# Kernel tuning notes

Hardware: AMD Instinct MI355X
Metric: run time of the kernel (lower is better)

## Reference

```python
import jax, jax.numpy as jnp
import numpy as np


def _quant8(w):
    # Brevitas Int8 per-tensor weight quant: scale = max|w|/127, round, clip, dequant.
    s = jnp.max(jnp.abs(w)) / 127.0
    q = jnp.clip(jnp.round(w / s), -127.0, 127.0) * s
    # straight-through estimator (matches brevitas backward)
    return w + jax.lax.stop_gradient(q - w)


def _conv1d(x, w, b):
    # x: [B, Cin, L], w: [Cout, Cin, K]
    y = jax.lax.conv_general_dilated(x, w, window_strides=(1,), padding='VALID',
                                     dimension_numbers=('NCW', 'OIW', 'NCW'))
    return y + b[None, :, None]


def _maxpool2(x):
    B, C, L = x.shape
    L2 = L // 2
    return jnp.max(x[:, :, :2 * L2].reshape(B, C, L2, 2), axis=-1)


def _lrelu(x):
    return jnp.where(x > 0, x, 0.1 * x)


def setup_inputs() -> dict:
    key = jax.random.key(0)
    ks = jax.random.split(key, 13)
    B, C, L = 32768, 2, 128
    flat = 32 * 27  # 864, from tracing conv/pool stack at L=128
    d = {
        'x': jax.random.normal(ks[0], (B, C, L), dtype=jnp.float32),
        'w1': jax.random.normal(ks[1], (16, 2, 2), dtype=jnp.float32) * 0.3,
        'b1': jax.random.normal(ks[2], (16,), dtype=jnp.float32) * 0.05,
        'w2': jax.random.normal(ks[3], (16, 16, 3), dtype=jnp.float32) * 0.1,
        'b2': jax.random.normal(ks[4], (16,), dtype=jnp.float32) * 0.05,
        'w3': jax.random.normal(ks[5], (32, 16, 5), dtype=jnp.float32) * 0.1,
        'b3': jax.random.normal(ks[6], (32,), dtype=jnp.float32) * 0.05,
        'w4': jax.random.normal(ks[7], (32, 32, 5), dtype=jnp.float32) * 0.08,
        'b4': jax.random.normal(ks[8], (32,), dtype=jnp.float32) * 0.05,
        'wd': jax.random.normal(ks[9], (64, flat), dtype=jnp.float32) * 0.03,
        'bd': jax.random.normal(ks[10], (64,), dtype=jnp.float32) * 0.05,
        'wo': jax.random.normal(ks[11], (1, 64), dtype=jnp.float32) * 0.1,
        'bo': jax.random.normal(ks[12], (1,), dtype=jnp.float32) * 0.05,
    }
    return d


def reference(x, w1, b1, w2, b2, w3, b3, w4, b4, wd, bd, wo, bo):
    h = _lrelu(_conv1d(x, _quant8(w1), b1))        # [B,16,127]
    h = _lrelu(_conv1d(h, _quant8(w2), b2))        # [B,16,125]
    h = _maxpool2(h)                               # [B,16,62]
    h = _lrelu(_conv1d(h, _quant8(w3), b3))        # [B,32,58]
    h = _lrelu(_conv1d(h, _quant8(w4), b4))        # [B,32,54]
    h = _maxpool2(h)                               # [B,32,27]
    h = h.reshape(h.shape[0], -1)                  # [B,864]
    h = _lrelu(h @ _quant8(wd).T + bd)             # [B,64]
    return h @ _quant8(wo).T + bo                  # [B,1]
```

## Files before the change

### kernel.cpp

```cpp
#include <hip/hip_runtime.h>
#include <hip/hip_bf16.h>

typedef __hip_bfloat16 bf16;
typedef _Float16 h16;
typedef __attribute__((ext_vector_type(8))) _Float16 h16x8;
typedef __attribute__((ext_vector_type(4))) float f32x4;
typedef __attribute__((ext_vector_type(16))) float f32x16;

__device__ __forceinline__ float lrelu(float x) { return x > 0.f ? x : 0.1f * x; }
__device__ __forceinline__ float ldE(const void* p, long i, int f32) {
    return f32 ? ((const float*)p)[i] : __bfloat162float(((const bf16*)p)[i]);
}
__device__ __forceinline__ uint2 pack4(float a, float b, float c, float d) {
    union { _Float16 h[4]; uint2 u; } t;
    t.h[0] = (_Float16)a; t.h[1] = (_Float16)b; t.h[2] = (_Float16)c; t.h[3] = (_Float16)d;
    return t.u;
}
#define LDS_FENCE() asm volatile("s_waitcnt lgkmcnt(0)" ::: "memory")


__device__ __forceinline__ float qv(const void* src, int idx, float sc, int f32) {
    float w = ldE(src, idx, f32);
    float q = rintf(w / sc);
    return fminf(127.f, fmaxf(-127.f, q)) * sc;
}

__global__ void __launch_bounds__(256) quant_prep(
    const unsigned short* __restrict__ xu,
    const void* __restrict__ w1, const void* __restrict__ w2,
    const void* __restrict__ w3, const void* __restrict__ w4,
    const void* __restrict__ wd, const void* __restrict__ wo,
    const void* __restrict__ b1, const void* __restrict__ b2,
    const void* __restrict__ b3, const void* __restrict__ b4,
    const void* __restrict__ bd, const void* __restrict__ bo,
    float* __restrict__ wsf)
{
    int tid = threadIdx.x;
    int which = blockIdx.x;
    __shared__ float red[256];
    __shared__ int cnt;
    if (tid == 0) cnt = 0;
    __syncthreads();
    int bad = 0;
    for (int i = tid; i < 2048; i += 256) {
        int e = (xu[i] >> 7) & 0xFF;
        if (e >= 147) bad = 1;
    }
    atomicAdd(&cnt, bad);
    __syncthreads();
    const int f32 = (cnt > 4) ? 1 : 0;
    if (tid == 0) ((int*)wsf)[290] = f32;

    h16* wh = (h16*)(wsf + 292);

    if (which == 53) {
        if (tid < 16)        wsf[64 + tid]        = ldE(b1, tid, f32);
        else if (tid < 32)   wsf[80 + tid - 16]   = ldE(b2, tid - 16, f32);
        else if (tid < 64)   wsf[96 + tid - 32]   = ldE(b3, tid - 32, f32);
        else if (tid < 96)   wsf[128 + tid - 64]  = ldE(b4, tid - 64, f32);
        else if (tid < 160)  wsf[160 + tid - 96]  = ldE(bd, tid - 96, f32);
        else if (tid == 160) wsf[288]             = ldE(bo, 0, f32);
        return;
    }

    if (which < 48) {
        float m0 = 0.f, m1 = 0.f, m2 = 0.f, m3 = 0.f;
        for (int i = tid; i < 55296; i += 1024) {
            m0 = fmaxf(m0, fabsf(ldE(wd, i, f32)));
            m1 = fmaxf(m1, fabsf(ldE(wd, i + 256, f32)));
            m2 = fmaxf(m2, fabsf(ldE(wd, i + 512, f32)));
            m3 = fmaxf(m3, fabsf(ldE(wd, i + 768, f32)));
        }
        red[tid] = fmaxf(fmaxf(m0, m1), fmaxf(m2, m3));
        __syncthreads();
        for (int s = 128; s > 0; s >>= 1) {
            if (tid < s) red[tid] = fmaxf(red[tid], red[tid + s]);
            __syncthreads();
        }
        float sc = red[0] / 127.f;
        int e1 = (which + 1) * 1152;
        for (int e = which * 1152 + tid; e < e1; e += 256) {
            int j = e & 7, l = (e >> 3) & 63, t = e >> 9;
            int mt = t / 27, c = t - mt * 27;
            int o = mt * 16 + (l & 15);
            int k = c * 32 + ((l >> 4) & 3) * 8 + j;
            int i = k >> 5, cch = k & 31;
            wh[8704 + e] = (h16)qv(wd, o * 864 + cch * 27 + i, sc, f32);
        }
        return;
    }

    const void* src; int n;
    switch (which) {
        case 48: src = w1; n = 64;   break;
        case 49: src = w2; n = 768;  break;
        case 50: src = w3; n = 2560; break;
        case 51: src = w4; n = 5120; break;
        default: src = wo; n = 64;   break;
    }
    float m = 0.f;
    for (int i = tid; i < n; i += 256) m = fmaxf(m, fabsf(ldE(src, i, f32)));
    red[tid] = m;
    __syncthreads();
    for (int s = 128; s > 0; s >>= 1) {
        if (tid < s) red[tid] = fmaxf(red[tid], red[tid + s]);
        __syncthreads();
    }
    float sc = red[0] / 127.f;

    if (which == 48) {
        if (tid < 64) wsf[tid] = qv(src, tid, sc, f32);
    } else if (which == 52) {
        if (tid < 64) wsf[224 + tid] = qv(src, tid, sc, f32);
    } else if (which == 49) {
        for (int e = tid; e < 1024; e += 256) {
            int c = e >> 9, l = (e >> 3) & 63, j = e & 7;
            int mm = l & 15;
            int k = c * 32 + ((l >> 4) & 3) * 8 + j;
            int dk = k >> 4, ci = k & 15;
            float v = (dk < 3) ? qv(src, (mm * 16 + ci) * 3 + dk, sc, f32) : 0.f;
            wh[0 + e] = (h16)v;
        }
    } else if (which == 50) {
        for (int e = tid; e < 2560; e += 256) {
            int c = e >> 9, l = (e >> 3) & 63, j = e & 7;
            int mm = l & 31;
            int ci = ((l >> 5) & 1) * 8 + j;
            wh[1024 + e] = (h16)qv(src, (mm * 16 + ci) * 5 + c, sc, f32);
        }
    } else {
        for (int e = tid; e < 5120; e += 256) {
            int c = e >> 9, l = (e >> 3) & 63, j = e & 7;
            int mm = l & 31;
            int k = c * 16 + ((l >> 5) & 1) * 8 + j;
            int dk = k >> 5, ci = k & 31;
            wh[3584 + e] = (h16)qv(src, (mm * 32 + ci) * 5 + dk, sc, f32);
        }
    }
}

__global__ void __launch_bounds__(256, 3) qcnn_main(
    const void* __restrict__ x,
    const float* __restrict__ wsf,
    void* __restrict__ out)
{
    const int f32flag = ((const int*)wsf)[290];
    const float* qw1f = wsf;
    const float* fb1g = wsf + 64;
    const h16*  wh  = (const h16*)(wsf + 292);
    const h16*  F2g = wh;
    const h16*  F3g = wh + 1024;
    const h16*  F4g = wh + 3584;
    const h16*  FDg = wh + 8704;

    __shared__ __align__(16) h16 Uall[4][2112];
    __shared__ __align__(16) h16 Vall[4][2208];
    __shared__ __align__(16) h16 flatb[8][872];
    __shared__ float red[256];

    int tid  = threadIdx.x;
    int lane = tid & 63;
    int w    = __builtin_amdgcn_readfirstlane(tid >> 6);
    int n16  = lane & 15, kg16 = (lane >> 4) & 3;
    int n32  = lane & 31, kg32 = (lane >> 5) & 1;
    int o16  = kg16 * 4;
    h16* U = Uall[w];
    h16* V = Vall[w];
    long b0 = (long)blockIdx.x * 8;

    h16x8 a2[2], a3[5], a4[10];
#pragma unroll
    for (int c = 0; c < 2; ++c)  a2[c] = *(const h16x8*)&F2g[c * 512 + lane * 8];
#pragma unroll
    for (int c = 0; c < 5; ++c)  a3[c] = *(const h16x8*)&F3g[c * 512 + lane * 8];
#pragma unroll
    for (int c = 0; c < 10; ++c) a4[c] = *(const h16x8*)&F4g[c * 512 + lane * 8];
    f32x4 b2v = *(const f32x4*)&wsf[80 + o16];

    for (int it = 0; it < 2; ++it) {
        int slot = w * 2 + it;
        long sb = (b0 + slot) * 256;

        LDS_FENCE();
        float xl[2][4];
#pragma unroll
        for (int ci = 0; ci < 2; ++ci) {
            int rb = ci * 128;
            xl[ci][0] = ldE(x, sb + rb + lane, f32flag);
            xl[ci][1] = ldE(x, sb + rb + lane + 1, f32flag);
            xl[ci][2] = ldE(x, sb + rb + 64 + lane, f32flag);
            xl[ci][3] = ldE(x, sb + rb + 64 + ((lane + 1) & 63), f32flag);
        }
        h16x8 ra, rbv, rc, rd;
#pragma unroll
        for (int co = 0; co < 16; ++co) {
            float w00 = qw1f[co*4+0], w01 = qw1f[co*4+1], w10 = qw1f[co*4+2], w11 = qw1f[co*4+3];
            float bb = fb1g[co];
            float v0 = bb + xl[0][0]*w00 + xl[0][1]*w01 + xl[1][0]*w10 + xl[1][1]*w11;
            float v1 = bb + xl[0][2]*w00 + xl[0][3]*w01 + xl[1][2]*w10 + xl[1][3]*w11;
            v0 = lrelu(v0); v1 = lrelu(v1);
            if (co < 8) { ra[co] = (h16)v0; rc[co] = (h16)v1; }
            else        { rbv[co-8] = (h16)v0; rd[co-8] = (h16)v1; }
        }
        *(h16x8*)&U[lane * 8]        = ra;
        *(h16x8*)&U[1056 + lane * 8] = rbv;
        if (lane < 63) {
            *(h16x8*)&U[(64 + lane) * 8]        = rc;
            *(h16x8*)&U[1056 + (64 + lane) * 8] = rd;
        }
        LDS_FENCE();

#pragma unroll
        for (int t = 0; t < 8; ++t) {
            int n = t * 16 + n16;
            f32x4 acc = {0.f, 0.f, 0.f, 0.f};
#pragma unroll
            for (int c = 0; c < 2; ++c) {
                int k0 = c * 32 + kg16 * 8;
                int dk = k0 >> 4, g = (k0 & 15) >> 3;
                h16x8 bfr = *(const h16x8*)&U[g * 1056 + (n + dk) * 8];
                acc = __builtin_amdgcn_mfma_f32_16x16x32_f16(a2[c], bfr, acc, 0, 0, 0);
            }
            if (n < 125) {
                uint2 p = pack4(lrelu(acc[0] + b2v[0]), lrelu(acc[1] + b2v[1]),
                                lrelu(acc[2] + b2v[2]), lrelu(acc[3] + b2v[3]));
                *(uint2*)&V[(o16 >> 3) * 1008 + n * 8 + (o16 & 7)] = p;
            }
        }
        LDS_FENCE();

        if (lane < 62) {
#pragma unroll
            for (int g = 0; g < 2; ++g) {
                h16x8 pa = *(const h16x8*)&V[g * 1008 + (2 * lane) * 8];
                h16x8 pb = *(const h16x8*)&V[g * 1008 + (2 * lane + 1) * 8];
                h16x8 mm;
#pragma unroll
                for (int e = 0; e < 8; ++e) mm[e] = pa[e] > pb[e] ? pa[e] : pb[e];
                *(h16x8*)&U[g * 1056 + lane * 8] = mm;
            }
        }
        LDS_FENCE();

#pragma unroll
        for (int t = 0; t < 2; ++t) {
            int n = t * 32 + n32;
            f32x16 acc = {0.f,0.f,0.f,0.f,0.f,0.f,0.f,0.f,0.f,0.f,0.f,0.f,0.f,0.f,0.f,0.f};
#pragma unroll
            for (int c = 0; c < 5; ++c) {
                h16x8 bfr = *(const h16x8*)&U[kg32 * 1056 + (n + c) * 8];
                acc = __builtin_amdgcn_mfma_f32_32x32x16_f16(a3[c], bfr, acc, 0, 0, 0);
            }
#pragma unroll
            for (int g = 0; g < 4; ++g) {
                int r0 = 8 * g + 4 * kg32;
                f32x4 bv = *(const f32x4*)&wsf[96 + r0];
                if (n < 58) {
                    uint2 p = pack4(lrelu(acc[4*g+0] + bv[0]), lrelu(acc[4*g+1] + bv[1]),
                                    lrelu(acc[4*g+2] + bv[2]), lrelu(acc[4*g+3] + bv[3]));
                    *(uint2*)&V[g * 552 + n * 8 + 4 * kg32] = p;
                }
            }
        }
        LDS_FENCE();

#pragma unroll
        for (int t = 0; t < 2; ++t) {
            int n = t * 32 + n32;
            f32x16 acc = {0.f,0.f,0.f,0.f,0.f,0.f,0.f,0.f,0.f,0.f,0.f,0.f,0.f,0.f,0.f,0.f};
#pragma unroll
            for (int c = 0; c < 10; ++c) {
                int k0 = c * 16 + kg32 * 8;
                int dk = k0 >> 5, g = (k0 >> 3) & 3;
                h16x8 bfr = *(const h16x8*)&V[g * 552 + (n + dk) * 8];
                acc = __builtin_amdgcn_mfma_f32_32x32x16_f16(a4[c], bfr, acc, 0, 0, 0);
            }
#pragma unroll
            for (int g = 0; g < 4; ++g) {
                int r0 = 8 * g + 4 * kg32;
                f32x4 bv = *(const f32x4*)&wsf[128 + r0];
                if (n < 54) {
                    uint2 p = pack4(lrelu(acc[4*g+0] + bv[0]), lrelu(acc[4*g+1] + bv[1]),
                                    lrelu(acc[4*g+2] + bv[2]), lrelu(acc[4*g+3] + bv[3]));
                    *(uint2*)&U[g * 448 + n * 8 + 4 * kg32] = p;
                }
            }
        }
        LDS_FENCE();

        if (lane < 27) {
#pragma unroll
            for (int g = 0; g < 4; ++g) {
                h16x8 pa = *(const h16x8*)&U[g * 448 + (2 * lane) * 8];
                h16x8 pb = *(const h16x8*)&U[g * 448 + (2 * lane + 1) * 8];
                h16x8 mm;
#pragma unroll
                for (int e = 0; e < 8; ++e) mm[e] = pa[e] > pb[e] ? pa[e] : pb[e];
                *(h16x8*)&flatb[slot][(g * 27 + lane) * 8] = mm;
            }
        }
    }
    __syncthreads();

    f32x4 dacc = {0.f, 0.f, 0.f, 0.f};
    for (int c = 0; c < 27; ++c) {
        h16x8 aw = *(const h16x8*)&FDg[((w * 27 + c) * 64 + lane) * 8];
        h16x8 bh = *(const h16x8*)&flatb[lane & 7][(kg16 * 27 + c) * 8];
        dacc = __builtin_amdgcn_mfma_f32_16x16x32_f16(aw, bh, dacc, 0, 0, 0);
    }
    int o0g = w * 16 + o16;
    f32x4 bdv = *(const f32x4*)&wsf[160 + o0g];
    f32x4 qov = *(const f32x4*)&wsf[224 + o0g];
    float part = 0.f;
#pragma unroll
    for (int q = 0; q < 4; ++q) part += lrelu(dacc[q] + bdv[q]) * qov[q];
    red[tid] = part;
    __syncthreads();
    if (tid < 8) {
        float y = wsf[288];
#pragma unroll
        for (int g = 0; g < 16; ++g) y += red[(g >> 2) * 64 + (g & 3) * 16 + tid];
        if (f32flag) ((float*)out)[b0 + tid] = y;
        else         ((bf16*)out)[b0 + tid] = __float2bfloat16(y);
    }
}

extern "C" void kernel_launch(void* const* d_in, const int* in_sizes, int n_in,
                              void* d_out, int out_size, void* d_ws, size_t ws_size,
                              hipStream_t stream) {
    const void* x  = d_in[0];
    const void* w1 = d_in[1];
    const void* b1 = d_in[2];
    const void* w2 = d_in[3];
    const void* b2 = d_in[4];
    const void* w3 = d_in[5];
    const void* b3 = d_in[6];
    const void* w4 = d_in[7];
    const void* b4 = d_in[8];
    const void* wd = d_in[9];
    const void* bd = d_in[10];
    const void* wo = d_in[11];
    const void* bo = d_in[12];
    float* wsf = (float*)d_ws;

    int B = in_sizes[0] / 256;
    quant_prep<<<54, 256, 0, stream>>>((const unsigned short*)x,
                                       w1, w2, w3, w4, wd, wo,
                                       b1, b2, b3, b4, bd, bo, wsf);
    qcnn_main<<<B / 8, 256, 0, stream>>>(x, wsf, d_out);
}
```

Before: 209.8 us.

## Fold biases into MFMA accumulators, preload inputs, and vectorize prep absmax

Initializes MFMA accumulators with the bias values so the per-element bias adds in the conv and dense epilogues go away. Rewrites leaky ReLU as a single fmax. Hoists the input loads for both iterations ahead of the loop so global latency overlaps. The prep kernel now computes absmax with vectorized integer bit-masking, and the w3/w4 quantization is split across more blocks. The costs are more live registers in the main kernel and redundant absmax reductions across the split prep blocks.

After: 214.9 us. 2.5% more time.

```diff
diff --git a/kernel.cpp b/kernel.cpp
--- a/kernel.cpp
+++ b/kernel.cpp
@@ -7,7 +7,7 @@
 typedef __attribute__((ext_vector_type(4))) float f32x4;
 typedef __attribute__((ext_vector_type(16))) float f32x16;
 
-__device__ __forceinline__ float lrelu(float x) { return x > 0.f ? x : 0.1f * x; }
+__device__ __forceinline__ float lrelu(float x) { return fmaxf(x, 0.1f * x); }
 __device__ __forceinline__ float ldE(const void* p, long i, int f32) {
     return f32 ? ((const float*)p)[i] : __bfloat162float(((const bf16*)p)[i]);
 }
@@ -16,6 +16,7 @@
     t.h[0] = (_Float16)a; t.h[1] = (_Float16)b; t.h[2] = (_Float16)c; t.h[3] = (_Float16)d;
     return t.u;
 }
+__device__ __forceinline__ unsigned umx(unsigned a, unsigned b) { return a > b ? a : b; }
 #define LDS_FENCE() asm volatile("s_waitcnt lgkmcnt(0)" ::: "memory")
 
 
@@ -25,7 +26,40 @@
     return fminf(127.f, fmaxf(-127.f, q)) * sc;
 }
 
-__global__ void __launch_bounds__(256) quant_prep(
+__device__ float block_scale(const void* src, int n, int f32, int tid, float* red) {
+    unsigned m = 0;
+    const uint4* p = (const uint4*)src;
+    if (f32) {
+        int nv = n >> 2;
+        for (int i = tid; i < nv; i += 256) {
+            uint4 u = p[i];
+            m = umx(m, u.x & 0x7FFFFFFFu); m = umx(m, u.y & 0x7FFFFFFFu);
+            m = umx(m, u.z & 0x7FFFFFFFu); m = umx(m, u.w & 0x7FFFFFFFu);
+        }
+        union { unsigned u; float f; } c; c.u = m;
+        red[tid] = c.f;
+    } else {
+        int nv = n >> 3;
+        for (int i = tid; i < nv; i += 256) {
+            uint4 u = p[i];
+            unsigned a;
+            a = u.x & 0x7FFF7FFFu; m = umx(m, a >> 16); m = umx(m, a & 0xFFFFu);
+            a = u.y & 0x7FFF7FFFu; m = umx(m, a >> 16); m = umx(m, a & 0xFFFFu);
+            a = u.z & 0x7FFF7FFFu; m = umx(m, a >> 16); m = umx(m, a & 0xFFFFu);
+            a = u.w & 0x7FFF7FFFu; m = umx(m, a >> 16); m = umx(m, a & 0xFFFFu);
+        }
+        union { unsigned u; float f; } c; c.u = m << 16;
+        red[tid] = c.f;
+    }
+    __syncthreads();
+    for (int s = 128; s > 0; s >>= 1) {
+        if (tid < s) red[tid] = fmaxf(red[tid], red[tid + s]);
+        __syncthreads();
+    }
+    return red[0] / 127.f;
+}
+
+__global__ void __launch_bounds__(256) prep(
     const unsigned short* __restrict__ xu,
     const void* __restrict__ w1, const void* __restrict__ w2,
     const void* __restrict__ w3, const void* __restrict__ w4,
@@ -35,8 +69,7 @@
     const void* __restrict__ bd, const void* __restrict__ bo,
     float* __restrict__ wsf)
 {
-    int tid = threadIdx.x;
-    int which = blockIdx.x;
+    int tid = threadIdx.x, which = blockIdx.x;
     __shared__ float red[256];
     __shared__ int cnt;
     if (tid == 0) cnt = 0;
@@ -49,35 +82,10 @@
     atomicAdd(&cnt, bad);
     __syncthreads();
     const int f32 = (cnt > 4) ? 1 : 0;
-    if (tid == 0) ((int*)wsf)[290] = f32;
-
     h16* wh = (h16*)(wsf + 292);
 
-    if (which == 53) {
-        if (tid < 16)        wsf[64 + tid]        = ldE(b1, tid, f32);
-        else if (tid < 32)   wsf[80 + tid - 16]   = ldE(b2, tid - 16, f32);
-        else if (tid < 64)   wsf[96 + tid - 32]   = ldE(b3, tid - 32, f32);
-        else if (tid < 96)   wsf[128 + tid - 64]  = ldE(b4, tid - 64, f32);
-        else if (tid < 160)  wsf[160 + tid - 96]  = ldE(bd, tid - 96, f32);
-        else if (tid == 160) wsf[288]             = ldE(bo, 0, f32);
-        return;
-    }
-
     if (which < 48) {
-        float m0 = 0.f, m1 = 0.f, m2 = 0.f, m3 = 0.f;
-        for (int i = tid; i < 55296; i += 1024) {
-            m0 = fmaxf(m0, fabsf(ldE(wd, i, f32)));
-            m1 = fmaxf(m1, fabsf(ldE(wd, i + 256, f32)));
-            m2 = fmaxf(m2, fabsf(ldE(wd, i + 512, f32)));
-            m3 = fmaxf(m3, fabsf(ldE(wd, i + 768, f32)));
-        }
-        red[tid] = fmaxf(fmaxf(m0, m1), fmaxf(m2, m3));
-        __syncthreads();
-        for (int s = 128; s > 0; s >>= 1) {
-            if (tid < s) red[tid] = fmaxf(red[tid], red[tid + s]);
-            __syncthreads();
-        }
-        float sc = red[0] / 127.f;
+        float sc = block_scale(wd, 55296, f32, tid, red);
         int e1 = (which + 1) * 1152;
         for (int e = which * 1152 + tid; e < e1; e += 256) {
             int j = e & 7, l = (e >> 3) & 63, t = e >> 9;
@@ -87,55 +95,48 @@
             int i = k >> 5, cch = k & 31;
             wh[8704 + e] = (h16)qv(wd, o * 864 + cch * 27 + i, sc, f32);
         }
-        return;
-    }
-
-    const void* src; int n;
-    switch (which) {
-        case 48: src = w1; n = 64;   break;
-        case 49: src = w2; n = 768;  break;
-        case 50: src = w3; n = 2560; break;
-        case 51: src = w4; n = 5120; break;
-        default: src = wo; n = 64;   break;
-    }
-    float m = 0.f;
-    for (int i = tid; i < n; i += 256) m = fmaxf(m, fabsf(ldE(src, i, f32)));
-    red[tid] = m;
-    __syncthreads();
-    for (int s = 128; s > 0; s >>= 1) {
-        if (tid < s) red[tid] = fmaxf(red[tid], red[tid + s]);
-        __syncthreads();
-    }
-    float sc = red[0] / 127.f;
-
-    if (which == 48) {
-        if (tid < 64) wsf[tid] = qv(src, tid, sc, f32);
-    } else if (which == 52) {
-        if (tid < 64) wsf[224 + tid] = qv(src, tid, sc, f32);
+    } else if (which == 48) {
+        float sc = block_scale(w1, 64, f32, tid, red);
+        if (tid < 64) wsf[tid] = qv(w1, tid, sc, f32);
     } else if (which == 49) {
+        float sc = block_scale(w2, 768, f32, tid, red);
         for (int e = tid; e < 1024; e += 256) {
             int c = e >> 9, l = (e >> 3) & 63, j = e & 7;
             int mm = l & 15;
             int k = c * 32 + ((l >> 4) & 3) * 8 + j;
             int dk = k >> 4, ci = k & 15;
-            float v = (dk < 3) ? qv(src, (mm * 16 + ci) * 3 + dk, sc, f32) : 0.f;
+            float v = (dk < 3) ? qv(w2, (mm * 16 + ci) * 3 + dk, sc, f32) : 0.f;
             wh[0 + e] = (h16)v;
         }
-    } else if (which == 50) {
-        for (int e = tid; e < 2560; e += 256) {
+    } else if (which < 52) {
+        float sc = block_scale(w3, 2560, f32, tid, red);
+        int e0 = (which - 50) * 1280;
+        for (int e = e0 + tid; e < e0 + 1280; e += 256) {
             int c = e >> 9, l = (e >> 3) & 63, j = e & 7;
             int mm = l & 31;
             int ci = ((l >> 5) & 1) * 8 + j;
-            wh[1024 + e] = (h16)qv(src, (mm * 16 + ci) * 5 + c, sc, f32);
-        }
-    } else {
-        for (int e = tid; e < 5120; e += 256) {
+            wh[1024 + e] = (h16)qv(w3, (mm * 16 + ci) * 5 + c, sc, f32);
+        }
+    } else if (which < 56) {
+        float sc = block_scale(w4, 5120, f32, tid, red);
+        int e0 = (which - 52) * 1280;
+        for (int e = e0 + tid; e < e0 + 1280; e += 256) {
             int c = e >> 9, l = (e >> 3) & 63, j = e & 7;
             int mm = l & 31;
             int k = c * 16 + ((l >> 5) & 1) * 8 + j;
             int dk = k >> 5, ci = k & 31;
-            wh[3584 + e] = (h16)qv(src, (mm * 32 + ci) * 5 + dk, sc, f32);
-        }
+            wh[3584 + e] = (h16)qv(w4, (mm * 32 + ci) * 5 + dk, sc, f32);
+        }
+    } else {
+        float sc = block_scale(wo, 64, f32, tid, red);
+        if (tid < 64) wsf[224 + tid] = qv(wo, tid, sc, f32);
+        if (tid < 16)        wsf[64 + tid]        = ldE(b1, tid, f32);
+        else if (tid < 32)   wsf[80 + tid - 16]   = ldE(b2, tid - 16, f32);
+        else if (tid < 64)   wsf[96 + tid - 32]   = ldE(b3, tid - 32, f32);
+        else if (tid < 96)   wsf[128 + tid - 64]  = ldE(b4, tid - 64, f32);
+        else if (tid < 160)  wsf[160 + tid - 96]  = ldE(bd, tid - 96, f32);
+        else if (tid == 160) wsf[288]             = ldE(bo, 0, f32);
+        if (tid == 0) ((int*)wsf)[290] = f32;
     }
 }
 
@@ -176,28 +177,40 @@
 #pragma unroll
     for (int c = 0; c < 10; ++c) a4[c] = *(const h16x8*)&F4g[c * 512 + lane * 8];
     f32x4 b2v = *(const f32x4*)&wsf[80 + o16];
+    f32x16 c3i, c4i;
+#pragma unroll
+    for (int g = 0; g < 4; ++g) {
+        f32x4 bv3 = *(const f32x4*)&wsf[96 + 8 * g + 4 * kg32];
+        f32x4 bv4 = *(const f32x4*)&wsf[128 + 8 * g + 4 * kg32];
+#pragma unroll
+        for (int q = 0; q < 4; ++q) { c3i[4*g+q] = bv3[q]; c4i[4*g+q] = bv4[q]; }
+    }
+
+    float xl[2][2][4];
+#pragma unroll
+    for (int it = 0; it < 2; ++it) {
+        long sb = (b0 + w * 2 + it) * 256;
+#pragma unroll
+        for (int ci = 0; ci < 2; ++ci) {
+            int rb = ci * 128;
+            xl[it][ci][0] = ldE(x, sb + rb + lane, f32flag);
+            xl[it][ci][1] = ldE(x, sb + rb + lane + 1, f32flag);
+            xl[it][ci][2] = ldE(x, sb + rb + 64 + lane, f32flag);
+            xl[it][ci][3] = ldE(x, sb + rb + 64 + ((lane + 1) & 63), f32flag);
+        }
+    }
 
     for (int it = 0; it < 2; ++it) {
         int slot = w * 2 + it;
-        long sb = (b0 + slot) * 256;
-
-        LDS_FENCE();
-        float xl[2][4];
-#pragma unroll
-        for (int ci = 0; ci < 2; ++ci) {
-            int rb = ci * 128;
-            xl[ci][0] = ldE(x, sb + rb + lane, f32flag);
-            xl[ci][1] = ldE(x, sb + rb + lane + 1, f32flag);
-            xl[ci][2] = ldE(x, sb + rb + 64 + lane, f32flag);
-            xl[ci][3] = ldE(x, sb + rb + 64 + ((lane + 1) & 63), f32flag);
-        }
+
+        LDS_FENCE();
         h16x8 ra, rbv, rc, rd;
 #pragma unroll
         for (int co = 0; co < 16; ++co) {
             float w00 = qw1f[co*4+0], w01 = qw1f[co*4+1], w10 = qw1f[co*4+2], w11 = qw1f[co*4+3];
             float bb = fb1g[co];
-            float v0 = bb + xl[0][0]*w00 + xl[0][1]*w01 + xl[1][0]*w10 + xl[1][1]*w11;
-            float v1 = bb + xl[0][2]*w00 + xl[0][3]*w01 + xl[1][2]*w10 + xl[1][3]*w11;
+            float v0 = bb + xl[it][0][0]*w00 + xl[it][0][1]*w01 + xl[it][1][0]*w10 + xl[it][1][1]*w11;
+            float v1 = bb + xl[it][0][2]*w00 + xl[it][0][3]*w01 + xl[it][1][2]*w10 + xl[it][1][3]*w11;
             v0 = lrelu(v0); v1 = lrelu(v1);
             if (co < 8) { ra[co] = (h16)v0; rc[co] = (h16)v1; }
             else        { rbv[co-8] = (h16)v0; rd[co-8] = (h16)v1; }
@@ -213,7 +226,7 @@
 #pragma unroll
         for (int t = 0; t < 8; ++t) {
             int n = t * 16 + n16;
-            f32x4 acc = {0.f, 0.f, 0.f, 0.f};
+            f32x4 acc = b2v;
 #pragma unroll
             for (int c = 0; c < 2; ++c) {
                 int k0 = c * 32 + kg16 * 8;
@@ -222,8 +235,7 @@
                 acc = __builtin_amdgcn_mfma_f32_16x16x32_f16(a2[c], bfr, acc, 0, 0, 0);
             }
             if (n < 125) {
-                uint2 p = pack4(lrelu(acc[0] + b2v[0]), lrelu(acc[1] + b2v[1]),
-                                lrelu(acc[2] + b2v[2]), lrelu(acc[3] + b2v[3]));
+                uint2 p = pack4(lrelu(acc[0]), lrelu(acc[1]), lrelu(acc[2]), lrelu(acc[3]));
                 *(uint2*)&V[(o16 >> 3) * 1008 + n * 8 + (o16 & 7)] = p;
             }
         }
@@ -245,19 +257,17 @@
 #pragma unroll
         for (int t = 0; t < 2; ++t) {
             int n = t * 32 + n32;
-            f32x16 acc = {0.f,0.f,0.f,0.f,0.f,0.f,0.f,0.f,0.f,0.f,0.f,0.f,0.f,0.f,0.f,0.f};
+            f32x16 acc = c3i;
 #pragma unroll
             for (int c = 0; c < 5; ++c) {
                 h16x8 bfr = *(const h16x8*)&U[kg32 * 1056 + (n + c) * 8];
                 acc = __builtin_amdgcn_mfma_f32_32x32x16_f16(a3[c], bfr, acc, 0, 0, 0);
             }
-#pragma unroll
-            for (int g = 0; g < 4; ++g) {
-                int r0 = 8 * g + 4 * kg32;
-                f32x4 bv = *(const f32x4*)&wsf[96 + r0];
-                if (n < 58) {
-                    uint2 p = pack4(lrelu(acc[4*g+0] + bv[0]), lrelu(acc[4*g+1] + bv[1]),
-                                    lrelu(acc[4*g+2] + bv[2]), lrelu(acc[4*g+3] + bv[3]));
+            if (n < 58) {
+#pragma unroll
+                for (int g = 0; g < 4; ++g) {
+                    uint2 p = pack4(lrelu(acc[4*g+0]), lrelu(acc[4*g+1]),
+                                    lrelu(acc[4*g+2]), lrelu(acc[4*g+3]));
                     *(uint2*)&V[g * 552 + n * 8 + 4 * kg32] = p;
                 }
             }
@@ -267,7 +277,7 @@
 #pragma unroll
         for (int t = 0; t < 2; ++t) {
             int n = t * 32 + n32;
-            f32x16 acc = {0.f,0.f,0.f,0.f,0.f,0.f,0.f,0.f,0.f,0.f,0.f,0.f,0.f,0.f,0.f,0.f};
+            f32x16 acc = c4i;
 #pragma unroll
             for (int c = 0; c < 10; ++c) {
                 int k0 = c * 16 + kg32 * 8;
@@ -275,13 +285,11 @@
                 h16x8 bfr = *(const h16x8*)&V[g * 552 + (n + dk) * 8];
                 acc = __builtin_amdgcn_mfma_f32_32x32x16_f16(a4[c], bfr, acc, 0, 0, 0);
             }
-#pragma unroll
-            for (int g = 0; g < 4; ++g) {
-                int r0 = 8 * g + 4 * kg32;
-                f32x4 bv = *(const f32x4*)&wsf[128 + r0];
-                if (n < 54) {
-                    uint2 p = pack4(lrelu(acc[4*g+0] + bv[0]), lrelu(acc[4*g+1] + bv[1]),
-                                    lrelu(acc[4*g+2] + bv[2]), lrelu(acc[4*g+3] + bv[3]));
+            if (n < 54) {
+#pragma unroll
+                for (int g = 0; g < 4; ++g) {
+                    uint2 p = pack4(lrelu(acc[4*g+0]), lrelu(acc[4*g+1]),
+                                    lrelu(acc[4*g+2]), lrelu(acc[4*g+3]));
                     *(uint2*)&U[g * 448 + n * 8 + 4 * kg32] = p;
                 }
             }
@@ -302,18 +310,17 @@
     }
     __syncthreads();
 
-    f32x4 dacc = {0.f, 0.f, 0.f, 0.f};
+    int o0g = w * 16 + o16;
+    f32x4 dacc = *(const f32x4*)&wsf[160 + o0g];
     for (int c = 0; c < 27; ++c) {
         h16x8 aw = *(const h16x8*)&FDg[((w * 27 + c) * 64 + lane) * 8];
         h16x8 bh = *(const h16x8*)&flatb[lane & 7][(kg16 * 27 + c) * 8];
         dacc = __builtin_amdgcn_mfma_f32_16x16x32_f16(aw, bh, dacc, 0, 0, 0);
     }
-    int o0g = w * 16 + o16;
-    f32x4 bdv = *(const f32x4*)&wsf[160 + o0g];
     f32x4 qov = *(const f32x4*)&wsf[224 + o0g];
     float part = 0.f;
 #pragma unroll
-    for (int q = 0; q < 4; ++q) part += lrelu(dacc[q] + bdv[q]) * qov[q];
+    for (int q = 0; q < 4; ++q) part += lrelu(dacc[q]) * qov[q];
     red[tid] = part;
     __syncthreads();
     if (tid < 8) {
@@ -344,8 +351,8 @@
     float* wsf = (float*)d_ws;
 
     int B = in_sizes[0] / 256;
-    quant_prep<<<54, 256, 0, stream>>>((const unsigned short*)x,
-                                       w1, w2, w3, w4, wd, wo,
-                                       b1, b2, b3, b4, bd, bo, wsf);
+    prep<<<57, 256, 0, stream>>>((const unsigned short*)x,
+                                 w1, w2, w3, w4, wd, wo,
+                                 b1, b2, b3, b4, bd, bo, wsf);
     qcnn_main<<<B / 8, 256, 0, stream>>>(x, wsf, d_out);
 }
```
